# Kernel optimization log

Measured on AMD Instinct MI355X. Metric: run time of the kernel, lower is better.

## Reference

```python
import jax, jax.numpy as jnp
import numpy as np

B, S, H, KVH, D = 1, 2048, 32, 8, 128
ROPE_THETA = 500000.0


def _rotate_half(x):
    x1, x2 = jnp.split(x, 2, axis=-1)
    return jnp.concatenate((-x2, x1), axis=-1)


def setup_inputs() -> dict:
    key = jax.random.key(0)
    ks = jax.random.split(key, 5)
    hidden_states = jax.random.normal(ks[0], (B, S, H * D), dtype=jnp.float32)
    Wq = jax.random.normal(ks[1], (H * D, H * D), dtype=jnp.float32) * 0.02
    Wk = jax.random.normal(ks[2], (KVH * D, H * D), dtype=jnp.float32) * 0.02
    Wv = jax.random.normal(ks[3], (KVH * D, H * D), dtype=jnp.float32) * 0.02
    Wo = jax.random.normal(ks[4], (H * D, H * D), dtype=jnp.float32) * 0.02
    # rotary tables (Llama-style, concat of freqs with itself)
    inv_freq = 1.0 / (ROPE_THETA ** (jnp.arange(0, D, 2, dtype=jnp.float32) / D))
    freqs = jnp.arange(S, dtype=jnp.float32)[:, None] * inv_freq[None, :]  # [S, D/2]
    emb = jnp.concatenate((freqs, freqs), axis=-1)  # [S, D]
    cos = jnp.cos(emb)[None]  # [1, S, D]
    sin = jnp.sin(emb)[None]
    # additive causal mask, matching SDPA attn_mask semantics
    causal = jnp.tril(jnp.ones((S, S), dtype=bool))
    attention_mask = jnp.where(causal, 0.0, -1e9).astype(jnp.float32)[None, None]  # [1,1,S,S]
    return {"hidden_states": hidden_states, "attention_mask": attention_mask,
            "cos": cos, "sin": sin, "Wq": Wq, "Wk": Wk, "Wv": Wv, "Wo": Wo}


def reference(hidden_states, attention_mask, cos, sin, Wq, Wk, Wv, Wo):
    b, s, _ = hidden_states.shape
    d = cos.shape[-1]
    h = Wq.shape[0] // d
    kvh = Wk.shape[0] // d
    g = h // kvh  # GQA group size

    # fused QKV projection (nn.Linear: y = x @ W^T), then split heads -> [b, heads, s, d]
    q = jnp.einsum('bsi,oi->bso', hidden_states, Wq).reshape(b, s, h, d).transpose(0, 2, 1, 3)
    k = jnp.einsum('bsi,oi->bso', hidden_states, Wk).reshape(b, s, kvh, d).transpose(0, 2, 1, 3)
    v = jnp.einsum('bsi,oi->bso', hidden_states, Wv).reshape(b, s, kvh, d).transpose(0, 2, 1, 3)

    # rotary embedding (unsqueeze_dim=1)
    c = cos[:, None]  # [b,1,s,d]
    sn = sin[:, None]
    q = q * c + _rotate_half(q) * sn
    k = k * c + _rotate_half(k) * sn

    # GQA: view q as [b, kvh, g, s, d]; contract against un-repeated k/v
    qg = q.reshape(b, kvh, g, s, d)
    scale = 1.0 / jnp.sqrt(jnp.float32(d))
    scores = jnp.einsum('bkgsd,bktd->bkgst', qg, k) * scale  # [b,kvh,g,s,s]
    scores = scores + attention_mask[:, :, None]  # broadcast [b,1,1,s,s]
    probs = jax.nn.softmax(scores, axis=-1)
    attn = jnp.einsum('bkgst,bktd->bkgsd', probs, v)  # [b,kvh,g,s,d]

    attn = attn.reshape(b, h, s, d).transpose(0, 2, 1, 3).reshape(b, s, h * d)
    out = jnp.einsum('bso,po->bsp', attn, Wo)
    return out
```

## Files before the change

### kernel.cpp

```cpp
#include <hip/hip_runtime.h>
#include <hip/hip_bf16.h>

#define SEQ 2048
#define HD  128
#define NH  32
#define NKV 8
#define MODEL 4096
#define KVDIM 1024
#define QKVN 6144

typedef __attribute__((ext_vector_type(8))) short short8;
typedef __attribute__((ext_vector_type(4))) short short4v;
typedef __attribute__((ext_vector_type(4))) float float4v;

#define MFMA16(a, b, c) __builtin_amdgcn_mfma_f32_16x16x32_bf16(a, b, c, 0, 0, 0)

__device__ __forceinline__ short f2bf(float x) {
  unsigned u = __builtin_bit_cast(unsigned, x);
  u += 0x7fffu + ((u >> 16) & 1u);
  return (short)(u >> 16);
}
__device__ __forceinline__ float bf2f(short s) {
  unsigned u = ((unsigned)(unsigned short)s) << 16;
  return __builtin_bit_cast(float, u);
}

__device__ __forceinline__ void async_copy16(const void* g, void* l) {
  __builtin_amdgcn_global_load_lds((const __attribute__((address_space(1))) void*)g,
                                   (__attribute__((address_space(3))) void*)l, 16, 0, 0);
}

__global__ __launch_bounds__(256) void cast_fused(const float* __restrict__ wq,
                                                  const float* __restrict__ wk,
                                                  const float* __restrict__ wv,
                                                  const float* __restrict__ wo,
                                                  const float* __restrict__ hid,
                                                  short* __restrict__ dst) {
  int b = blockIdx.x;
  const float* src;
  int rbase, lblk;
  if (b < 16384)      { src = wq;  rbase = 0;     lblk = b; }
  else if (b < 20480) { src = wk;  rbase = 16384; lblk = b - 16384; }
  else if (b < 24576) { src = wv;  rbase = 20480; lblk = b - 20480; }
  else if (b < 40960) { src = wo;  rbase = 24576; lblk = b - 24576; }
  else                { src = hid; rbase = 40960; lblk = b - 40960; }
  size_t li = (size_t)lblk * 1024 + threadIdx.x * 4;
  float4v v = *(const float4v*)(src + li);
  short4v o;
  o[0] = f2bf(v[0]); o[1] = f2bf(v[1]); o[2] = f2bf(v[2]); o[3] = f2bf(v[3]);
  *(short4v*)(dst + (size_t)rbase * 1024 + li) = o;
}

__device__ __forceinline__ void store_out(float* C, size_t idx, float v) { C[idx] = v; }
__device__ __forceinline__ void store_out(short* C, size_t idx, float v) { C[idx] = f2bf(v); }

template <int NI, typename OUT>
__global__ __launch_bounds__(512, 2) void gemm256t(const short* __restrict__ A,
                                                   const short* __restrict__ B,
                                                   OUT* __restrict__ C,
                                                   int M, int N, int K) {
  constexpr int BN = NI * 64;
  __shared__ __align__(16) short As[2][256 * 64];
  __shared__ __align__(16) short Bs[2][BN * 64];
  const int tid = threadIdx.x;
  const int lane = tid & 63, w = tid >> 6;
  const int col = lane & 15, quad = lane >> 4;
  const int wm = w >> 2, wn = w & 3;

  const int nbx = N / BN;
  int bid = blockIdx.x, nwg = gridDim.x;
  int swz = (nwg & 7) ? bid : ((bid & 7) * (nwg >> 3) + (bid >> 3));
  const int m0 = (swz / nbx) << 8;
  const int n0 = (swz % nbx) * BN;

  const int srow = tid >> 3;
  const int schunk = (tid & 7) ^ (srow & 7);
  const short* pA = A + (size_t)(m0 + srow) * K + schunk * 8;
  const short* pB = B + (size_t)(n0 + srow) * K + schunk * 8;
  const int ldst = tid * 8;

  const int sw = (col & 7) << 3;
  const int kof0 = (quad * 8) ^ sw;
  const int kof1 = (32 + quad * 8) ^ sw;
  const int ra = wm * 128, rb = wn * (NI * 16);

  float4v acc[8][NI] = {};
  const int iters = K >> 6;

#define SA(buf, rA, kt) async_copy16(pA + (size_t)(rA) * K + (kt), &As[buf][(rA) * 64 + ldst])
#define SB_(buf, rB, kt) async_copy16(pB + (size_t)(rB) * K + (kt), &Bs[buf][(rB) * 64 + ldst])

  SA(0, 0, 0);  SA(0, 128, 0);
  SB_(0, 0, 0); SB_(0, 64, 0);
  if constexpr (NI == 3) SB_(0, 128, 0);
  SA(0, 64, 0); SA(0, 192, 0);
  asm volatile("s_waitcnt vmcnt(2)" ::: "memory");
  __builtin_amdgcn_s_barrier();

  for (int t = 0; t < iters; ++t) {
    const int cb = t & 1, nb = cb ^ 1;
    const int kt = (t + 1) << 6;
    const bool pf = (t + 1 < iters);
    const short* a_ = As[cb];
    const short* b_ = Bs[cb];
    short8 bf[NI][2];
    short8 af[4][2];

#pragma unroll
    for (int j = 0; j < 4; ++j) {
      const short* rp = a_ + (ra + j * 16 + col) * 64;
      af[j][0] = *(const short8*)(rp + kof0);
      af[j][1] = *(const short8*)(rp + kof1);
    }
#pragma unroll
    for (int ni = 0; ni < NI; ++ni) {
      const short* rp = b_ + (rb + ni * 16 + col) * 64;
      bf[ni][0] = *(const short8*)(rp + kof0);
      bf[ni][1] = *(const short8*)(rp + kof1);
    }
    if (pf) { SA(nb, 0, kt); SA(nb, 128, kt); SB_(nb, 0, kt); SB_(nb, 64, kt); }
    __builtin_amdgcn_s_barrier();
    asm volatile("s_waitcnt lgkmcnt(0)" ::: "memory");
    __builtin_amdgcn_sched_barrier(0);
    __builtin_amdgcn_s_setprio(1);
#pragma unroll
    for (int j = 0; j < 4; ++j)
#pragma unroll
      for (int ni = 0; ni < NI; ++ni) {
        acc[j][ni] = MFMA16(af[j][0], bf[ni][0], acc[j][ni]);
        acc[j][ni] = MFMA16(af[j][1], bf[ni][1], acc[j][ni]);
      }
    __builtin_amdgcn_s_setprio(0);
    if (pf) asm volatile("s_waitcnt vmcnt(4)" ::: "memory");
    else    asm volatile("s_waitcnt vmcnt(0)" ::: "memory");
    __builtin_amdgcn_s_barrier();

#pragma unroll
    for (int j = 0; j < 4; ++j) {
      const short* rp = a_ + (ra + (4 + j) * 16 + col) * 64;
      af[j][0] = *(const short8*)(rp + kof0);
      af[j][1] = *(const short8*)(rp + kof1);
    }
    if (pf) {
      if constexpr (NI == 3) SB_(nb, 128, kt);
      SA(nb, 64, kt); SA(nb, 192, kt);
    }
    __builtin_amdgcn_s_barrier();
    asm volatile("s_waitcnt lgkmcnt(0)" ::: "memory");
    __builtin_amdgcn_sched_barrier(0);
    __builtin_amdgcn_s_setprio(1);
#pragma unroll
    for (int j = 0; j < 4; ++j)
#pragma unroll
      for (int ni = 0; ni < NI; ++ni) {
        acc[4 + j][ni] = MFMA16(af[j][0], bf[ni][0], acc[4 + j][ni]);
        acc[4 + j][ni] = MFMA16(af[j][1], bf[ni][1], acc[4 + j][ni]);
      }
    __builtin_amdgcn_s_setprio(0);
    if (pf) asm volatile("s_waitcnt vmcnt(2)" ::: "memory");
    __builtin_amdgcn_s_barrier();
  }
#undef SA
#undef SB_

#pragma unroll
  for (int mi = 0; mi < 8; ++mi)
#pragma unroll
    for (int ni = 0; ni < NI; ++ni)
#pragma unroll
      for (int r = 0; r < 4; ++r) {
        int row = m0 + ra + mi * 16 + quad * 4 + r;
        int cc  = n0 + rb + ni * 16 + col;
        store_out(C, (size_t)row * N + cc, acc[mi][ni][r]);
      }
}

#define BM 128
#define BN 128
#define BK 32

template <typename OUT>
__global__ __launch_bounds__(256) void gemm_nt(const short* __restrict__ A,
                                               const short* __restrict__ B,
                                               OUT* __restrict__ C,
                                               int M, int N, int K) {
  __shared__ __align__(16) short As[2][BM * BK];
  __shared__ __align__(16) short Bs[2][BN * BK];
  int t = threadIdx.x;
  int w = t >> 6, lane = t & 63;
  int col = lane & 15, quad = lane >> 4;
  int m0 = blockIdx.y * BM, n0 = blockIdx.x * BN;
  int wr = (w >> 1) * 64, wc = (w & 1) * 64;

  int srow   = lane >> 2;
  int schunk = (lane & 3) ^ ((lane >> 3) & 3);
  const short* Ag0 = A + (size_t)(m0 + w * 32 + srow) * K + schunk * 8;
  const short* Ag1 = Ag0 + (size_t)16 * K;
  const short* Bg0 = B + (size_t)(n0 + w * 32 + srow) * K + schunk * 8;
  const short* Bg1 = Bg0 + (size_t)16 * K;
  const int wofs0 = (w * 32) * BK;
  const int wofs1 = (w * 32 + 16) * BK;

  int aswz = (quad ^ ((col >> 1) & 3)) * 8;

  float4v acc[4][4] = {};

  async_copy16(Ag0, &As[0][wofs0]);
  async_copy16(Ag1, &As[0][wofs1]);
  async_copy16(Bg0, &Bs[0][wofs0]);
  async_copy16(Bg1, &Bs[0][wofs1]);
  __syncthreads();

  const int iters = K / BK;
  for (int it = 0; it < iters; it++) {
    const int cb = it & 1, nb = cb ^ 1;
    if (it + 1 < iters) {
      const int k0 = (it + 1) * BK;
      async_copy16(Ag0 + k0, &As[nb][wofs0]);
      async_copy16(Ag1 + k0, &As[nb][wofs1]);
      async_copy16(Bg0 + k0, &Bs[nb][wofs0]);
      async_copy16(Bg1 + k0, &Bs[nb][wofs1]);
    }
    short8 af[4], bfr[4];
#pragma unroll
    for (int i = 0; i < 4; i++)
      af[i] = *(const short8*)&As[cb][(wr + i * 16 + col) * BK + aswz];
#pragma unroll
    for (int i = 0; i < 4; i++)
      bfr[i] = *(const short8*)&Bs[cb][(wc + i * 16 + col) * BK + aswz];
#pragma unroll
    for (int mi = 0; mi < 4; mi++)
#pragma unroll
      for (int ni = 0; ni < 4; ni++)
        acc[mi][ni] = MFMA16(af[mi], bfr[ni], acc[mi][ni]);
    __syncthreads();
  }

#pragma unroll
  for (int mi = 0; mi < 4; mi++)
#pragma unroll
    for (int ni = 0; ni < 4; ni++)
#pragma unroll
      for (int r = 0; r < 4; r++) {
        int row = m0 + wr + mi * 16 + quad * 4 + r;
        int cc  = n0 + wc + ni * 16 + col;
        store_out(C, (size_t)row * N + cc, acc[mi][ni][r]);
      }
}

__global__ __launch_bounds__(128) void rope_kernel(const short* __restrict__ qkv,
                                                   const float* __restrict__ cosp,
                                                   const float* __restrict__ sinp,
                                                   short* __restrict__ qb,
                                                   short* __restrict__ kb) {
  int s = blockIdx.x, head = blockIdx.y, d = threadIdx.x;
  float c  = cosp[s * HD + d];
  float sn = sinp[s * HD + d];
  if (head < NH) {
    const short* base = qkv + (size_t)s * QKVN + head * HD;
    float x = bf2f(base[d]);
    float rot = (d < 64) ? -bf2f(base[d + 64]) : bf2f(base[d - 64]);
    qb[((size_t)(head * SEQ + s)) * HD + d] = f2bf((x * c + rot * sn) * 0.08838834764831845f);
  } else {
    int hk = head - NH;
    const short* base = qkv + (size_t)s * QKVN + MODEL + hk * HD;
    float x = bf2f(base[d]);
    float rot = (d < 64) ? -bf2f(base[d + 64]) : bf2f(base[d - 64]);
    kb[((size_t)(hk * SEQ + s)) * HD + d] = f2bf(x * c + rot * sn);
  }
}

__global__ __launch_bounds__(256) void vtrans_kernel(const short* __restrict__ qkv,
                                                     short* __restrict__ vt) {
  __shared__ short tile[32][34];
  int kv = blockIdx.z;
  int d0 = blockIdx.x * 32, s0 = blockIdx.y * 32;
  int tx = threadIdx.x, ty = threadIdx.y;
#pragma unroll
  for (int j = 0; j < 32; j += 8)
    tile[ty + j][tx] = qkv[(size_t)(s0 + ty + j) * QKVN + MODEL + KVDIM + kv * HD + d0 + tx];
  __syncthreads();
#pragma unroll
  for (int j = 0; j < 32; j += 8)
    vt[((size_t)(kv * HD + d0 + ty + j)) * SEQ + s0 + tx] = tile[tx][ty + j];
}

#define FKT 32
#define KLD 136
#define VLD 40
#define PLD 40

__global__ __launch_bounds__(256, 3) void flash_attn(const short* __restrict__ qb_,
                                                     const short* __restrict__ kb,
                                                     const short* __restrict__ vt,
                                                     short* __restrict__ attn) {
  __shared__ __align__(16) short Ks[2][FKT * KLD];
  __shared__ __align__(16) short Vs[2][HD * VLD];
  __shared__ __align__(16) short Ps[4][32 * PLD];
  const int tid = threadIdx.x;
  const int w = tid >> 6, lane = tid & 63;
  const int col = lane & 15, quad = lane >> 4;
  const int h = blockIdx.x;
  const int kv = h >> 2;
  const int yp = (blockIdx.y < 8) ? (15 - (int)blockIdx.y) : ((int)blockIdx.y - 8);
  const int qB0 = yp * 128;
  const int q0w = qB0 + w * 32;
  const int ntiles = qB0 / FKT + 4;

  short8 ones;
#pragma unroll
  for (int i = 0; i < 8; i++) ones[i] = (short)0x3F80;

  short8 qf[2][4];
  const short* qbase = qb_ + ((size_t)(h * SEQ + q0w + col)) * HD;
#pragma unroll
  for (int rt = 0; rt < 2; rt++)
#pragma unroll
    for (int ks = 0; ks < 4; ks++)
      qf[rt][ks] = *(const short8*)(qbase + rt * 16 * HD + ks * 32 + quad * 8);

  float4v o[2][8] = {};
  float4v la[2] = {};

  const int kg_off = tid * 8;
  const int klds0  = (kg_off >> 7) * KLD + (kg_off & 127);
  const int vd     = tid >> 2;
  const int vkof   = (tid & 3) * 8;
  const size_t vrow0 = ((size_t)(kv * HD + vd)) * SEQ;
  const size_t vrow1 = ((size_t)(kv * HD + vd + 64)) * SEQ;
  const int vlds0 = vd * VLD + vkof;
  const short* kgbase = kb + ((size_t)kv * SEQ) * HD;

  short8 kr0, kr1, vr0, vr1;
  kr0 = *(const short8*)(kgbase + kg_off);
  kr1 = *(const short8*)(kgbase + 2048 + kg_off);
  vr0 = *(const short8*)(vt + vrow0 + vkof);
  vr1 = *(const short8*)(vt + vrow1 + vkof);
  *(short8*)&Ks[0][klds0]            = kr0;
  *(short8*)&Ks[0][klds0 + 16 * KLD] = kr1;
  *(short8*)&Vs[0][vlds0]            = vr0;
  *(short8*)&Vs[0][vlds0 + 64 * VLD] = vr1;
  __syncthreads();

  for (int kt = 0; kt < ntiles; kt++) {
    const int b = kt & 1;
    const int key0 = kt * FKT;
    if (kt + 1 < ntiles) {
      const int nk0 = key0 + FKT;
      const short* kg = kgbase + (size_t)nk0 * HD;
      kr0 = *(const short8*)(kg + kg_off);
      kr1 = *(const short8*)(kg + 2048 + kg_off);
      vr0 = *(const short8*)(vt + vrow0 + nk0 + vkof);
      vr1 = *(const short8*)(vt + vrow1 + nk0 + vkof);
    }
    if (key0 <= q0w + 31) {
      float4v sct[2][2] = {};
#pragma unroll
      for (int ks = 0; ks < 4; ks++) {
        short8 kf0 = *(const short8*)&Ks[b][col * KLD + ks * 32 + quad * 8];
        short8 kf1 = *(const short8*)&Ks[b][(16 + col) * KLD + ks * 32 + quad * 8];
        sct[0][0] = MFMA16(kf0, qf[0][ks], sct[0][0]);
        sct[0][1] = MFMA16(kf0, qf[1][ks], sct[0][1]);
        sct[1][0] = MFMA16(kf1, qf[0][ks], sct[1][0]);
        sct[1][1] = MFMA16(kf1, qf[1][ks], sct[1][1]);
      }
      short* pw = Ps[w];
#pragma unroll
      for (int rt = 0; rt < 2; rt++) {
        int qrow = q0w + rt * 16 + col;
#pragma unroll
        for (int kt2 = 0; kt2 < 2; kt2++) {
          int keyb = key0 + kt2 * 16 + quad * 4;
          short4v p;
#pragma unroll
          for (int r = 0; r < 4; r++) {
            float s = sct[kt2][rt][r];
            if (keyb + r > qrow) s = -INFINITY;
            p[r] = f2bf(__expf(s));
          }
          *(short4v*)&pw[(rt * 16 + col) * PLD + kt2 * 16 + quad * 4] = p;
        }
      }
      asm volatile("s_waitcnt lgkmcnt(0)" ::: "memory");
      short8 pf0 = *(const short8*)&pw[col * PLD + quad * 8];
      short8 pf1 = *(const short8*)&pw[(16 + col) * PLD + quad * 8];
      la[0] = MFMA16(ones, pf0, la[0]);
      la[1] = MFMA16(ones, pf1, la[1]);
#pragma unroll
      for (int nc = 0; nc < 8; nc++) {
        short8 vb = *(const short8*)&Vs[b][(nc * 16 + col) * VLD + quad * 8];
        o[0][nc] = MFMA16(vb, pf0, o[0][nc]);
        o[1][nc] = MFMA16(vb, pf1, o[1][nc]);
      }
    }
    if (kt + 1 < ntiles) {
      const int nb = 1 - b;
      *(short8*)&Ks[nb][klds0]            = kr0;
      *(short8*)&Ks[nb][klds0 + 16 * KLD] = kr1;
      *(short8*)&Vs[nb][vlds0]            = vr0;
      *(short8*)&Vs[nb][vlds0 + 64 * VLD] = vr1;
    }
    __syncthreads();
  }

#pragma unroll
  for (int rt = 0; rt < 2; rt++) {
    float inv = 1.0f / la[rt][0];
    size_t rowbase = (size_t)(q0w + rt * 16 + col) * MODEL + h * HD + quad * 4;
#pragma unroll
    for (int nc = 0; nc < 8; nc++) {
      short4v ov;
#pragma unroll
      for (int r = 0; r < 4; r++) ov[r] = f2bf(o[rt][nc][r] * inv);
      *(short4v*)(attn + rowbase + nc * 16) = ov;
    }
  }
}

extern "C" void kernel_launch(void* const* d_in, const int* in_sizes, int n_in,
                              void* d_out, int out_size, void* d_ws, size_t ws_size,
                              hipStream_t stream) {
  const float* hidden = (const float*)d_in[0];
  const float* cosp = (const float*)d_in[2];
  const float* sinp = (const float*)d_in[3];
  const float* Wq   = (const float*)d_in[4];
  const float* Wk   = (const float*)d_in[5];
  const float* Wv   = (const float*)d_in[6];
  const float* Wo   = (const float*)d_in[7];

  char* ws = (char*)d_ws;
  size_t off = 0;
  auto alloc = [&](size_t bytes) {
    char* p = ws + off;
    off += (bytes + 255) & ~(size_t)255;
    return p;
  };
  short* wq_bf = (short*)alloc((size_t)MODEL * MODEL * 2);
  short* wk_bf = (short*)alloc((size_t)KVDIM * MODEL * 2);
  short* wv_bf = (short*)alloc((size_t)KVDIM * MODEL * 2);
  short* wo_bf = (short*)alloc((size_t)MODEL * MODEL * 2);
  short* h_bf  = (short*)alloc((size_t)SEQ * MODEL * 2);
  short* qkv_bf = (short*)alloc((size_t)SEQ * QKVN * 2);
  short* k_bf  = (short*)alloc((size_t)NKV * SEQ * HD * 2);
  short* v_t   = (short*)alloc((size_t)NKV * HD * SEQ * 2);
  short* attn_bf = (short*)alloc((size_t)SEQ * MODEL * 2);
  short* q_bf    = h_bf;

  cast_fused<<<49152, 256, 0, stream>>>(Wq, Wk, Wv, Wo, hidden, wq_bf);

  gemm256t<3, short><<<dim3((SEQ / 256) * (QKVN / 192)), 512, 0, stream>>>(
      h_bf, wq_bf, qkv_bf, SEQ, QKVN, MODEL);

  rope_kernel<<<dim3(SEQ, NH + NKV), 128, 0, stream>>>(qkv_bf, cosp, sinp, q_bf, k_bf);
  vtrans_kernel<<<dim3(HD / 32, SEQ / 32, NKV), dim3(32, 8), 0, stream>>>(qkv_bf, v_t);

  flash_attn<<<dim3(NH, SEQ / 128), 256, 0, stream>>>(q_bf, k_bf, v_t, attn_bf);

  gemm_nt<float><<<dim3(MODEL / BN, SEQ / BM), 256, 0, stream>>>(
      attn_bf, wo_bf, (float*)d_out, SEQ, MODEL, MODEL);
}
```

Measured before the change: 518.7 us.

## Split GEMM k-step into four phases and drop LDS staging in flash attention

The QKV GEMM main loop now runs as four half-size phases instead of two, with fewer A fragments held per phase and the async global-to-LDS prefetches spread across the phases. The flash attention kernel drops the shared K/V double buffers and the block-wide __syncthreads. Each wave now loads its K and V fragments straight from global memory, so it only walks its own causal range. This removes block synchronisation and LDS traffic, but each of the four waves reads the same K/V from global/L2 with no reuse, and raised register pressure lowers the occupancy hint from 3 to 2.

```diff
diff --git a/kernel.cpp b/kernel.cpp
--- a/kernel.cpp
+++ b/kernel.cpp
@@ -55,7 +55,7 @@
 __device__ __forceinline__ void store_out(short* C, size_t idx, float v) { C[idx] = f2bf(v); }
 
 template <int NI, typename OUT>
-__global__ __launch_bounds__(512, 2) void gemm256t(const short* __restrict__ A,
+__global__ __launch_bounds__(512, 2) void gemm256v(const short* __restrict__ A,
                                                    const short* __restrict__ B,
                                                    OUT* __restrict__ C,
                                                    int M, int N, int K) {
@@ -104,10 +104,10 @@
     const short* a_ = As[cb];
     const short* b_ = Bs[cb];
     short8 bf[NI][2];
-    short8 af[4][2];
-
-#pragma unroll
-    for (int j = 0; j < 4; ++j) {
+    short8 af[2][2];
+
+#pragma unroll
+    for (int j = 0; j < 2; ++j) {
       const short* rp = a_ + (ra + j * 16 + col) * 64;
       af[j][0] = *(const short8*)(rp + kof0);
       af[j][1] = *(const short8*)(rp + kof1);
@@ -118,43 +118,82 @@
       bf[ni][0] = *(const short8*)(rp + kof0);
       bf[ni][1] = *(const short8*)(rp + kof1);
     }
-    if (pf) { SA(nb, 0, kt); SA(nb, 128, kt); SB_(nb, 0, kt); SB_(nb, 64, kt); }
+    if (pf) { SA(nb, 0, kt); SA(nb, 128, kt); }
     __builtin_amdgcn_s_barrier();
     asm volatile("s_waitcnt lgkmcnt(0)" ::: "memory");
     __builtin_amdgcn_sched_barrier(0);
     __builtin_amdgcn_s_setprio(1);
 #pragma unroll
-    for (int j = 0; j < 4; ++j)
+    for (int j = 0; j < 2; ++j)
 #pragma unroll
       for (int ni = 0; ni < NI; ++ni) {
         acc[j][ni] = MFMA16(af[j][0], bf[ni][0], acc[j][ni]);
         acc[j][ni] = MFMA16(af[j][1], bf[ni][1], acc[j][ni]);
       }
     __builtin_amdgcn_s_setprio(0);
+    __builtin_amdgcn_s_barrier();
+
+#pragma unroll
+    for (int j = 0; j < 2; ++j) {
+      const short* rp = a_ + (ra + (2 + j) * 16 + col) * 64;
+      af[j][0] = *(const short8*)(rp + kof0);
+      af[j][1] = *(const short8*)(rp + kof1);
+    }
+    if (pf) { SB_(nb, 0, kt); SB_(nb, 64, kt); }
+    __builtin_amdgcn_s_barrier();
+    asm volatile("s_waitcnt lgkmcnt(0)" ::: "memory");
+    __builtin_amdgcn_sched_barrier(0);
+    __builtin_amdgcn_s_setprio(1);
+#pragma unroll
+    for (int j = 0; j < 2; ++j)
+#pragma unroll
+      for (int ni = 0; ni < NI; ++ni) {
+        acc[2 + j][ni] = MFMA16(af[j][0], bf[ni][0], acc[2 + j][ni]);
+        acc[2 + j][ni] = MFMA16(af[j][1], bf[ni][1], acc[2 + j][ni]);
+      }
+    __builtin_amdgcn_s_setprio(0);
     if (pf) asm volatile("s_waitcnt vmcnt(4)" ::: "memory");
     else    asm volatile("s_waitcnt vmcnt(0)" ::: "memory");
     __builtin_amdgcn_s_barrier();
 
 #pragma unroll
-    for (int j = 0; j < 4; ++j) {
+    for (int j = 0; j < 2; ++j) {
       const short* rp = a_ + (ra + (4 + j) * 16 + col) * 64;
       af[j][0] = *(const short8*)(rp + kof0);
       af[j][1] = *(const short8*)(rp + kof1);
     }
-    if (pf) {
-      if constexpr (NI == 3) SB_(nb, 128, kt);
-      SA(nb, 64, kt); SA(nb, 192, kt);
-    }
+    if (pf) { if constexpr (NI == 3) SB_(nb, 128, kt); }
     __builtin_amdgcn_s_barrier();
     asm volatile("s_waitcnt lgkmcnt(0)" ::: "memory");
     __builtin_amdgcn_sched_barrier(0);
     __builtin_amdgcn_s_setprio(1);
 #pragma unroll
-    for (int j = 0; j < 4; ++j)
+    for (int j = 0; j < 2; ++j)
 #pragma unroll
       for (int ni = 0; ni < NI; ++ni) {
         acc[4 + j][ni] = MFMA16(af[j][0], bf[ni][0], acc[4 + j][ni]);
         acc[4 + j][ni] = MFMA16(af[j][1], bf[ni][1], acc[4 + j][ni]);
+      }
+    __builtin_amdgcn_s_setprio(0);
+    __builtin_amdgcn_s_barrier();
+
+#pragma unroll
+    for (int j = 0; j < 2; ++j) {
+      const short* rp = a_ + (ra + (6 + j) * 16 + col) * 64;
+      af[j][0] = *(const short8*)(rp + kof0);
+      af[j][1] = *(const short8*)(rp + kof1);
+    }
+    if (pf) { SA(nb, 64, kt); SA(nb, 192, kt); }
+    __builtin_amdgcn_s_barrier();
+    asm volatile("s_waitcnt lgkmcnt(0)" ::: "memory");
+    __builtin_amdgcn_sched_barrier(0);
+    __builtin_amdgcn_s_setprio(1);
+#pragma unroll
+    for (int j = 0; j < 2; ++j)
+#pragma unroll
+      for (int ni = 0; ni < NI; ++ni) {
+        acc[6 + j][ni] = MFMA16(af[j][0], bf[ni][0], acc[6 + j][ni]);
+        acc[6 + j][ni] = MFMA16(af[j][1], bf[ni][1], acc[6 + j][ni]);
       }
     __builtin_amdgcn_s_setprio(0);
     if (pf) asm volatile("s_waitcnt vmcnt(2)" ::: "memory");
@@ -285,17 +324,12 @@
     vt[((size_t)(kv * HD + d0 + ty + j)) * SEQ + s0 + tx] = tile[tx][ty + j];
 }
 
-#define FKT 32
-#define KLD 136
-#define VLD 40
 #define PLD 40
 
-__global__ __launch_bounds__(256, 3) void flash_attn(const short* __restrict__ qb_,
+__global__ __launch_bounds__(256, 2) void flash_attn(const short* __restrict__ qb_,
                                                      const short* __restrict__ kb,
                                                      const short* __restrict__ vt,
                                                      short* __restrict__ attn) {
-  __shared__ __align__(16) short Ks[2][FKT * KLD];
-  __shared__ __align__(16) short Vs[2][HD * VLD];
   __shared__ __align__(16) short Ps[4][32 * PLD];
   const int tid = threadIdx.x;
   const int w = tid >> 6, lane = tid & 63;
@@ -305,7 +339,7 @@
   const int yp = (blockIdx.y < 8) ? (15 - (int)blockIdx.y) : ((int)blockIdx.y - 8);
   const int qB0 = yp * 128;
   const int q0w = qB0 + w * 32;
-  const int ntiles = qB0 / FKT + 4;
+  const int wtiles = (q0w + 31) >> 5;
 
   short8 ones;
 #pragma unroll
@@ -322,85 +356,61 @@
   float4v o[2][8] = {};
   float4v la[2] = {};
 
-  const int kg_off = tid * 8;
-  const int klds0  = (kg_off >> 7) * KLD + (kg_off & 127);
-  const int vd     = tid >> 2;
-  const int vkof   = (tid & 3) * 8;
-  const size_t vrow0 = ((size_t)(kv * HD + vd)) * SEQ;
-  const size_t vrow1 = ((size_t)(kv * HD + vd + 64)) * SEQ;
-  const int vlds0 = vd * VLD + vkof;
   const short* kgbase = kb + ((size_t)kv * SEQ) * HD;
-
-  short8 kr0, kr1, vr0, vr1;
-  kr0 = *(const short8*)(kgbase + kg_off);
-  kr1 = *(const short8*)(kgbase + 2048 + kg_off);
-  vr0 = *(const short8*)(vt + vrow0 + vkof);
-  vr1 = *(const short8*)(vt + vrow1 + vkof);
-  *(short8*)&Ks[0][klds0]            = kr0;
-  *(short8*)&Ks[0][klds0 + 16 * KLD] = kr1;
-  *(short8*)&Vs[0][vlds0]            = vr0;
-  *(short8*)&Vs[0][vlds0 + 64 * VLD] = vr1;
-  __syncthreads();
-
-  for (int kt = 0; kt < ntiles; kt++) {
-    const int b = kt & 1;
-    const int key0 = kt * FKT;
-    if (kt + 1 < ntiles) {
-      const int nk0 = key0 + FKT;
-      const short* kg = kgbase + (size_t)nk0 * HD;
-      kr0 = *(const short8*)(kg + kg_off);
-      kr1 = *(const short8*)(kg + 2048 + kg_off);
-      vr0 = *(const short8*)(vt + vrow0 + nk0 + vkof);
-      vr1 = *(const short8*)(vt + vrow1 + nk0 + vkof);
-    }
-    if (key0 <= q0w + 31) {
-      float4v sct[2][2] = {};
-#pragma unroll
-      for (int ks = 0; ks < 4; ks++) {
-        short8 kf0 = *(const short8*)&Ks[b][col * KLD + ks * 32 + quad * 8];
-        short8 kf1 = *(const short8*)&Ks[b][(16 + col) * KLD + ks * 32 + quad * 8];
-        sct[0][0] = MFMA16(kf0, qf[0][ks], sct[0][0]);
-        sct[0][1] = MFMA16(kf0, qf[1][ks], sct[0][1]);
-        sct[1][0] = MFMA16(kf1, qf[0][ks], sct[1][0]);
-        sct[1][1] = MFMA16(kf1, qf[1][ks], sct[1][1]);
-      }
-      short* pw = Ps[w];
-#pragma unroll
-      for (int rt = 0; rt < 2; rt++) {
-        int qrow = q0w + rt * 16 + col;
-#pragma unroll
-        for (int kt2 = 0; kt2 < 2; kt2++) {
-          int keyb = key0 + kt2 * 16 + quad * 4;
-          short4v p;
-#pragma unroll
-          for (int r = 0; r < 4; r++) {
-            float s = sct[kt2][rt][r];
-            if (keyb + r > qrow) s = -INFINITY;
-            p[r] = f2bf(__expf(s));
-          }
-          *(short4v*)&pw[(rt * 16 + col) * PLD + kt2 * 16 + quad * 4] = p;
+  const short* vgbase = vt + ((size_t)kv * HD) * SEQ;
+  short* pw = Ps[w];
+
+  for (int kt = 0; kt <= wtiles; kt++) {
+    const int key0 = kt * 32;
+    short8 vb[8];
+#pragma unroll
+    for (int nc = 0; nc < 8; nc++)
+      vb[nc] = *(const short8*)(vgbase + (size_t)(nc * 16 + col) * SEQ + key0 + quad * 8);
+    short8 kf0[4], kf1[4];
+    const short* kg = kgbase + (size_t)(key0 + col) * HD + quad * 8;
+#pragma unroll
+    for (int ks = 0; ks < 4; ks++) {
+      kf0[ks] = *(const short8*)(kg + ks * 32);
+      kf1[ks] = *(const short8*)(kg + 16 * HD + ks * 32);
+    }
+    float4v sct[2][2] = {};
+    __builtin_amdgcn_s_setprio(1);
+#pragma unroll
+    for (int ks = 0; ks < 4; ks++) {
+      sct[0][0] = MFMA16(kf0[ks], qf[0][ks], sct[0][0]);
+      sct[0][1] = MFMA16(kf0[ks], qf[1][ks], sct[0][1]);
+      sct[1][0] = MFMA16(kf1[ks], qf[0][ks], sct[1][0]);
+      sct[1][1] = MFMA16(kf1[ks], qf[1][ks], sct[1][1]);
+    }
+    __builtin_amdgcn_s_setprio(0);
+#pragma unroll
+    for (int rt = 0; rt < 2; rt++) {
+      int qrow = q0w + rt * 16 + col;
+#pragma unroll
+      for (int kt2 = 0; kt2 < 2; kt2++) {
+        int keyb = key0 + kt2 * 16 + quad * 4;
+        short4v p;
+#pragma unroll
+        for (int r = 0; r < 4; r++) {
+          float s = sct[kt2][rt][r];
+          if (keyb + r > qrow) s = -INFINITY;
+          p[r] = f2bf(__expf(s));
         }
-      }
-      asm volatile("s_waitcnt lgkmcnt(0)" ::: "memory");
-      short8 pf0 = *(const short8*)&pw[col * PLD + quad * 8];
-      short8 pf1 = *(const short8*)&pw[(16 + col) * PLD + quad * 8];
-      la[0] = MFMA16(ones, pf0, la[0]);
-      la[1] = MFMA16(ones, pf1, la[1]);
-#pragma unroll
-      for (int nc = 0; nc < 8; nc++) {
-        short8 vb = *(const short8*)&Vs[b][(nc * 16 + col) * VLD + quad * 8];
-        o[0][nc] = MFMA16(vb, pf0, o[0][nc]);
-        o[1][nc] = MFMA16(vb, pf1, o[1][nc]);
-      }
-    }
-    if (kt + 1 < ntiles) {
-      const int nb = 1 - b;
-      *(short8*)&Ks[nb][klds0]            = kr0;
-      *(short8*)&Ks[nb][klds0 + 16 * KLD] = kr1;
-      *(short8*)&Vs[nb][vlds0]            = vr0;
-      *(short8*)&Vs[nb][vlds0 + 64 * VLD] = vr1;
-    }
-    __syncthreads();
+        *(short4v*)&pw[(rt * 16 + col) * PLD + kt2 * 16 + quad * 4] = p;
+      }
+    }
+    asm volatile("s_waitcnt lgkmcnt(0)" ::: "memory");
+    short8 pf0 = *(const short8*)&pw[col * PLD + quad * 8];
+    short8 pf1 = *(const short8*)&pw[(16 + col) * PLD + quad * 8];
+    __builtin_amdgcn_s_setprio(1);
+    la[0] = MFMA16(ones, pf0, la[0]);
+    la[1] = MFMA16(ones, pf1, la[1]);
+#pragma unroll
+    for (int nc = 0; nc < 8; nc++) {
+      o[0][nc] = MFMA16(vb[nc], pf0, o[0][nc]);
+      o[1][nc] = MFMA16(vb[nc], pf1, o[1][nc]);
+    }
+    __builtin_amdgcn_s_setprio(0);
   }
 
 #pragma unroll
@@ -448,7 +458,7 @@
 
   cast_fused<<<49152, 256, 0, stream>>>(Wq, Wk, Wv, Wo, hidden, wq_bf);
 
-  gemm256t<3, short><<<dim3((SEQ / 256) * (QKVN / 192)), 512, 0, stream>>>(
+  gemm256v<3, short><<<dim3((SEQ / 256) * (QKVN / 192)), 512, 0, stream>>>(
       h_bf, wq_bf, qkv_bf, SEQ, QKVN, MODEL);
 
   rope_kernel<<<dim3(SEQ, NH + NKV), 128, 0, stream>>>(qkv_bf, cosp, sinp, q_bf, k_bf);
```

New measurement: 577.4 us. 11.3% more time.
